# Performance work log

Hardware: AMD Instinct MI355X
Metric: run time of the kernel (lower is better)

## Reference

```python
import math
import jax, jax.numpy as jnp
import numpy as np

D_MODEL = 256
NUM_HEAD = 8
NUM_LEVEL = 1
KERNEL = 5
NUM_POINT = KERNEL * KERNEL
NUM_VAR = 5  # with_rotation=True
HEAD_DIM = D_MODEL // NUM_HEAD


def _kernel_indices(k=KERNEL):
    # odd kernel: linspace(-(k-1)/2, (k-1)/2, k); torch.meshgrid default 'ij'; stack([j,i])/k
    idx = jnp.linspace(-(k - 1) / 2.0, (k - 1) / 2.0, k)
    ii, jj = jnp.meshgrid(idx, idx, indexing='ij')
    return jnp.stack([jj, ii], axis=-1).reshape(-1, 2) / k  # (P, 2)


def setup_inputs() -> dict:
    key = jax.random.key(0)
    ks = jax.random.split(key, 8)
    B, LQ = 2, 4096
    Hf, Wf = 188, 188
    LV = Hf * Wf
    d = D_MODEL
    nb = NUM_LEVEL * NUM_HEAD * NUM_VAR
    na = NUM_HEAD * NUM_LEVEL * NUM_POINT
    return {
        'query': jax.random.normal(ks[0], (B, LQ, d), jnp.float32),
        'value': jax.random.normal(ks[1], (B, LV, d), jnp.float32),
        'ref_windows': jax.random.uniform(ks[2], (B, LQ, 7), jnp.float32),
        'W_box': jax.random.normal(ks[3], (nb, d), jnp.float32) * 0.02,
        'b_box': jax.random.uniform(ks[4], (nb,), jnp.float32),
        'W_attn': jax.random.normal(ks[5], (na, d), jnp.float32) * 0.02,
        'b_attn': jnp.zeros((na,), jnp.float32),
        'W_value': jax.random.normal(ks[6], (d, d), jnp.float32) * 0.02,
        'b_value': jnp.zeros((d,), jnp.float32),
        'W_out': jax.random.normal(ks[7], (d, d), jnp.float32) * 0.02,
        'b_out': jnp.zeros((d,), jnp.float32),
        'H_feat': Hf,
        'W_feat': Wf,
    }


def reference(query, value, ref_windows, W_box, b_box, W_attn, b_attn,
              W_value, b_value, W_out, b_out, H_feat, W_feat):
    B, LQ, d = query.shape
    LV = value.shape[1]
    Hh, Lv, P, Dh = NUM_HEAD, NUM_LEVEL, NUM_POINT, HEAD_DIM

    # value projection -> (B, LV, Hh, Dh)
    v = (value @ W_value.T + b_value).reshape(B, LV, Hh, Dh)

    # attention weights: softmax over (level*point) per head
    attn = jax.nn.softmax((query @ W_attn.T + b_attn).reshape(B, LQ, Hh, Lv * P), axis=-1)
    attn = attn.reshape(B, LQ, Hh, Lv, P)

    # --- _where_to_attend ---
    ob = (query @ W_box.T + b_box).reshape(B, LQ, Hh, Lv, NUM_VAR)
    rw = ref_windows[:, :, None, None, :]                    # (B,LQ,1,1,7)
    ref_boxes = rw[..., jnp.array([0, 1, 3, 4])]             # cx, cy, w, h
    ref_angles = rw[..., 6:7]
    off_boxes, off_angles = ob[..., :4], ob[..., 4:5]
    angles = (ref_angles + off_angles / 16.0) * (2.0 * math.pi)
    boxes = ref_boxes + off_boxes / 8.0 * ref_boxes[..., jnp.array([2, 3, 2, 3])]
    center = boxes[..., None, :2]                            # (B,LQ,Hh,Lv,1,2)
    size = boxes[..., None, 2:4]
    cos_a, sin_a = jnp.cos(angles), jnp.sin(angles)
    rot = jnp.stack([cos_a, -sin_a, sin_a, cos_a], axis=-1).reshape(B, LQ, Hh, Lv, 1, 2, 2)
    g = _kernel_indices() * jax.nn.relu(size)                # (B,LQ,Hh,Lv,P,2)
    grid = center + (g[..., None, :] * rot).sum(-1)          # (B,LQ,Hh,Lv,P,2), normalized [0,1]

    # --- single-level bilinear sampling (align_corners=False, zero padding) ---
    gl = grid[:, :, :, 0]                                    # (B,LQ,Hh,P,2)
    gx = gl[..., 0] * W_feat - 0.5
    gy = gl[..., 1] * H_feat - 0.5
    x0 = jnp.floor(gx)
    y0 = jnp.floor(gy)
    x0i = x0.astype(jnp.int32)
    y0i = y0.astype(jnp.int32)
    wx1 = gx - x0
    wy1 = gy - y0
    wx0 = 1.0 - wx1
    wy0 = 1.0 - wy1

    b_idx = jnp.arange(B)[:, None, None, None]
    h_idx = jnp.arange(Hh)[None, None, :, None]

    def gather(yi, xi):
        valid = (xi >= 0) & (xi < W_feat) & (yi >= 0) & (yi < H_feat)
        lin = jnp.clip(yi, 0, H_feat - 1) * W_feat + jnp.clip(xi, 0, W_feat - 1)
        return v[b_idx, lin, h_idx] * valid[..., None]       # (B,LQ,Hh,P,Dh)

    s = (gather(y0i, x0i) * (wy0 * wx0)[..., None]
         + gather(y0i, x0i + 1) * (wy0 * wx1)[..., None]
         + gather(y0i + 1, x0i) * (wy1 * wx0)[..., None]
         + gather(y0i + 1, x0i + 1) * (wy1 * wx1)[..., None])

    out_heads = (s * attn[:, :, :, 0, :, None]).sum(axis=3)  # (B,LQ,Hh,Dh)
    out = out_heads.reshape(B, LQ, Hh * Dh) @ W_out.T + b_out
    attn_w = attn.reshape(B, LQ, Hh, Lv, KERNEL, KERNEL)
    return out, attn_w
```

## Files before the change

### kernel.cpp

```cpp
#include <hip/hip_runtime.h>


typedef float floatx4 __attribute__((ext_vector_type(4)));
typedef short shortx8 __attribute__((ext_vector_type(8)));

static __device__ __forceinline__ unsigned short f2bf(float x) {
    unsigned int u = __float_as_uint(x);
    return (unsigned short)((u + 0x7fffu + ((u >> 16) & 1u)) >> 16);
}
static __device__ __forceinline__ unsigned int pack2(float a, float b) {
    return (unsigned int)f2bf(a) | ((unsigned int)f2bf(b) << 16);
}
static __device__ __forceinline__ void async16(const void* g, void* lds) {
    __builtin_amdgcn_global_load_lds(
        (const __attribute__((address_space(1))) unsigned int*)g,
        (__attribute__((address_space(3))) unsigned int*)lds, 16, 0, 0);
}

__global__ __launch_bounds__(256) void convert_kernel(
    const float* __restrict__ W_value, unsigned short* __restrict__ wvbf,
    const float* __restrict__ W_attn, const float* __restrict__ W_box,
    float* __restrict__ Wab,
    const float* __restrict__ W_out, unsigned short* __restrict__ wobf,
    const float* __restrict__ b_attn, const float* __restrict__ b_box,
    float* __restrict__ bab)
{
    const int blk = blockIdx.x, tid = threadIdx.x;
    if (blk < 16) {
        int base = blk * 1024 + tid;
#pragma unroll
        for (int k = 0; k < 4; ++k) {
            int j = base + k * 256;
            float4 f = ((const float4*)W_value)[j];
            ((uint2*)wvbf)[j] = make_uint2(pack2(f.x, f.y), pack2(f.z, f.w));
        }
    } else if (blk < 32) {
        int base = (blk - 16) * 1024 + tid;
#pragma unroll
        for (int k = 0; k < 4; ++k) {
            int j = base + k * 256;
            int row = j >> 6, col = (j & 63) * 4;
            float4 f;
            if (row < 200)      f = *(const float4*)(W_attn + (size_t)row * 256 + col);
            else if (row < 240) f = *(const float4*)(W_box + (size_t)(row - 200) * 256 + col);
            else                f = make_float4(0.f, 0.f, 0.f, 0.f);
            ((float4*)Wab)[j] = f;
        }
    } else if (blk < 48) {
        int base = (blk - 32) * 1024 + tid;
#pragma unroll
        for (int k = 0; k < 4; ++k) {
            int j = base + k * 256;
            float4 f = ((const float4*)W_out)[j];
            ((uint2*)wobf)[j] = make_uint2(pack2(f.x, f.y), pack2(f.z, f.w));
        }
    } else {
        bab[tid] = tid < 200 ? b_attn[tid] : (tid < 240 ? b_box[tid - 200] : 0.f);
    }
}

__global__ __launch_bounds__(512) void gemm_vproj(
    const float* __restrict__ A,
    const unsigned short* __restrict__ Bw,
    const float* __restrict__ bias,
    unsigned short* __restrict__ Vout, int M, int LV)
{
    __shared__ unsigned short Bs[256 * 264];
    const int tid = threadIdx.x;
    const int wv = tid >> 6, lane = tid & 63;
    const int lr = lane & 15, lq = lane >> 4;
    const int wn = wv & 3, wm = wv >> 2;

#pragma unroll
    for (int it = 0; it < 16; ++it) {
        int j = it * 512 + tid;
        int row = j >> 5, gc = j & 31;
        uint4 v = *(const uint4*)(Bw + (size_t)row * 256 + gc * 8);
        *(uint4*)((char*)Bs + row * 528 + gc * 16) = v;
    }
    __syncthreads();

    int bbase[4];
#pragma unroll
    for (int t = 0; t < 4; ++t) {
        int rb = wn * 64 + t * 16 + lr;
        bbase[t] = rb * 528 + lq * 16;
    }

    const int niter = (M + 63) / 64;
    for (int it = blockIdx.x; it < niter; it += gridDim.x) {
        const float* ap[2];
#pragma unroll
        for (int t = 0; t < 2; ++t) {
            int ra = it * 64 + wm * 32 + t * 16 + lr;
            ra = ra < M ? ra : M - 1;
            ap[t] = A + (size_t)ra * 256 + lq * 8;
        }
        floatx4 acc[2][4];
#pragma unroll
        for (int i = 0; i < 2; ++i)
#pragma unroll
            for (int j = 0; j < 4; ++j) acc[i][j] = (floatx4){0.f, 0.f, 0.f, 0.f};

#pragma unroll
        for (int ks = 0; ks < 8; ++ks) {
            shortx8 af[2], bf[4];
#pragma unroll
            for (int t = 0; t < 4; ++t)
                bf[t] = *(const shortx8*)((const char*)Bs + bbase[t] + ks * 64);
#pragma unroll
            for (int t = 0; t < 2; ++t) {
                float4 f0 = *(const float4*)(ap[t] + ks * 32);
                float4 f1 = *(const float4*)(ap[t] + ks * 32 + 4);
                union { uint4 u; shortx8 s; } cv;
                cv.u = make_uint4(pack2(f0.x, f0.y), pack2(f0.z, f0.w),
                                  pack2(f1.x, f1.y), pack2(f1.z, f1.w));
                af[t] = cv.s;
            }
#pragma unroll
            for (int ti = 0; ti < 2; ++ti)
#pragma unroll
                for (int tj = 0; tj < 4; ++tj)
                    acc[ti][tj] = __builtin_amdgcn_mfma_f32_16x16x32_bf16(bf[tj], af[ti], acc[ti][tj], 0, 0, 0);
        }
#pragma unroll
        for (int ti = 0; ti < 2; ++ti) {
            int m = it * 64 + wm * 32 + ti * 16 + lr;
            if (m >= M) continue;
            int b = m >= LV ? 1 : 0;
            int lv = m - (b ? LV : 0);
#pragma unroll
            for (int tj = 0; tj < 4; ++tj) {
                int nb = wn * 64 + tj * 16 + lq * 4;
                float4 bv = *(const float4*)(bias + nb);
                int h = nb >> 5, dh = nb & 31;
                unsigned short* dst = Vout + ((size_t)(b * 8 + h) * LV + lv) * 32 + dh;
                *(uint2*)dst = make_uint2(pack2(acc[ti][tj][0] + bv.x, acc[ti][tj][1] + bv.y),
                                          pack2(acc[ti][tj][2] + bv.z, acc[ti][tj][3] + bv.w));
            }
        }
    }
}

__global__ __launch_bounds__(256) void gemm_out(
    const unsigned short* __restrict__ Ab,
    const unsigned short* __restrict__ Bw,
    const float* __restrict__ bias,
    float* __restrict__ C, int M)
{
    constexpr int BM = 64;
    constexpr int NI = BM / 32, TI = BM / 32;
    __shared__ unsigned short As[2][BM * 64];
    __shared__ unsigned short Bs[2][128 * 64];
    const int tid = threadIdx.x;
    const int wv = tid >> 6, lane = tid & 63;
    const int lr = lane & 15, lq = lane >> 4;
    const int m0 = blockIdx.x * BM, n0 = blockIdx.y * 128;
    const int wm = wv & 1, wn = wv >> 1;
    const int srow = tid >> 3;
    const int colg = tid & 7;
    const int colgSw = colg ^ (srow & 7);

    floatx4 acc[TI][4];
#pragma unroll
    for (int i = 0; i < TI; ++i)
#pragma unroll
        for (int j = 0; j < 4; ++j) acc[i][j] = (floatx4){0.f, 0.f, 0.f, 0.f};

    auto compute = [&](const unsigned short* Acur, const unsigned short* Bcur) {
#pragma unroll
        for (int kb = 0; kb < 2; ++kb) {
            shortx8 af[TI], bfr[4];
#pragma unroll
            for (int t = 0; t < TI; ++t) {
                int arow = wm * (BM / 2) + t * 16 + lr;
                af[t] = *(const shortx8*)&Acur[arow * 64 + (((kb * 4 + lq) ^ (arow & 7)) * 8)];
            }
#pragma unroll
            for (int t = 0; t < 4; ++t) {
                int brow = wn * 64 + t * 16 + lr;
                bfr[t] = *(const shortx8*)&Bcur[brow * 64 + (((kb * 4 + lq) ^ (brow & 7)) * 8)];
            }
#pragma unroll
            for (int ti = 0; ti < TI; ++ti)
#pragma unroll
                for (int tj = 0; tj < 4; ++tj)
                    acc[ti][tj] = __builtin_amdgcn_mfma_f32_16x16x32_bf16(bfr[tj], af[ti], acc[ti][tj], 0, 0, 0);
        }
    };

#pragma unroll
    for (int i = 0; i < NI; ++i) {
        int ra = m0 + i * 32 + srow; ra = ra < M ? ra : M - 1;
        async16(Ab + (size_t)ra * 256 + colgSw * 8, (char*)As[0] + i * 4096 + wv * 1024);
    }
#pragma unroll
    for (int i = 0; i < 4; ++i) {
        int rb = n0 + i * 32 + srow;
        async16(Bw + (size_t)rb * 256 + colgSw * 8, (char*)Bs[0] + i * 4096 + wv * 1024);
    }
    __syncthreads();
    int cur = 0;
    for (int kc = 0; kc < 4; ++kc) {
        const int nk = (kc + 1) * 64;
        if (kc < 3) {
#pragma unroll
            for (int i = 0; i < NI; ++i) {
                int ra = m0 + i * 32 + srow; ra = ra < M ? ra : M - 1;
                async16(Ab + (size_t)ra * 256 + nk + colgSw * 8,
                        (char*)As[cur ^ 1] + i * 4096 + wv * 1024);
            }
#pragma unroll
            for (int i = 0; i < 4; ++i) {
                int rb = n0 + i * 32 + srow;
                async16(Bw + (size_t)rb * 256 + nk + colgSw * 8,
                        (char*)Bs[cur ^ 1] + i * 4096 + wv * 1024);
            }
        }
        compute(As[cur], Bs[cur]);
        __syncthreads();
        cur ^= 1;
    }
#pragma unroll
    for (int ti = 0; ti < TI; ++ti) {
        int m = m0 + wm * (BM / 2) + ti * 16 + lr;
        if (m >= M) continue;
        float* Crow = C + (size_t)m * 256;
#pragma unroll
        for (int tj = 0; tj < 4; ++tj) {
            int nb = n0 + wn * 64 + tj * 16 + lq * 4;
            float4 bv = *(const float4*)(bias + nb);
            float4 o = make_float4(acc[ti][tj][0] + bv.x, acc[ti][tj][1] + bv.y,
                                   acc[ti][tj][2] + bv.z, acc[ti][tj][3] + bv.w);
            *(float4*)(Crow + nb) = o;
        }
    }
}

__global__ __launch_bounds__(256) void gemm_nt_bias(
    const float* __restrict__ A, const float* __restrict__ W,
    const float* __restrict__ bias, float* __restrict__ C, int M)
{
    const int K = 256, N = 256;
    __shared__ float As[16][68];
    __shared__ float Bs[16][68];
    int tid = threadIdx.x;
    int tcol = tid & 15, trow = tid >> 4;
    int m0 = blockIdx.x * 64, n0 = blockIdx.y * 64;
    int lr = tid >> 2, lc = (tid & 3) << 2;
    float acc[4][4] = {};
    for (int k0 = 0; k0 < K; k0 += 16) {
        int arow = m0 + lr; if (arow > M - 1) arow = M - 1;
        float4 av = *(const float4*)(A + (size_t)arow * K + k0 + lc);
        float4 wv = *(const float4*)(W + (size_t)(n0 + lr) * K + k0 + lc);
        __syncthreads();
        As[lc + 0][lr] = av.x; As[lc + 1][lr] = av.y; As[lc + 2][lr] = av.z; As[lc + 3][lr] = av.w;
        Bs[lc + 0][lr] = wv.x; Bs[lc + 1][lr] = wv.y; Bs[lc + 2][lr] = wv.z; Bs[lc + 3][lr] = wv.w;
        __syncthreads();
#pragma unroll
        for (int k = 0; k < 16; ++k) {
            float4 a4 = *(const float4*)&As[k][trow << 2];
            float4 b4 = *(const float4*)&Bs[k][tcol << 2];
            float a[4] = {a4.x, a4.y, a4.z, a4.w};
            float bb[4] = {b4.x, b4.y, b4.z, b4.w};
#pragma unroll
            for (int i = 0; i < 4; i++)
#pragma unroll
                for (int j = 0; j < 4; j++) acc[i][j] += a[i] * bb[j];
        }
    }
#pragma unroll
    for (int i = 0; i < 4; i++) {
        int m = m0 + trow * 4 + i;
        if (m >= M) continue;
#pragma unroll
        for (int j = 0; j < 4; j++) {
            int n = n0 + tcol * 4 + j;
            C[(size_t)m * N + n] = acc[i][j] + bias[n];
        }
    }
}

__global__ __launch_bounds__(256) void decode_sample_kernel(
    const unsigned short* __restrict__ v,
    const float* __restrict__ logits,
    const float* __restrict__ ref_windows,
    float* __restrict__ attn_out,
    unsigned short* __restrict__ ohbf,
    const int* __restrict__ Hf_p, const int* __restrict__ Wf_p, int LV, int LQ)
{
    __shared__ float lg[8][32];
    __shared__ float rw[8][7];
    __shared__ float prm[8][6];
    __shared__ float mxinv[8][2];
    __shared__ uint4 pk[8][25][2];

    const int lin = blockIdx.y * 16 + blockIdx.x;
    const int nc = gridDim.y;
    const int seq = lin >> 3;
    const int c = seq % nc;
    const int s = (lin & 7) + ((seq / nc) << 3);
    const int b = s >> 3, h = s & 7;
    const int tid = threadIdx.x;
    const int Hf = *Hf_p, Wf = *Wf_p;
    const size_t mbase = (size_t)b * LQ + c * 8;

    if (tid < 240) {
        int qq = tid / 30, j = tid - qq * 30;
        int col = (j < 25) ? h * 25 + j : 200 + h * 5 + (j - 25);
        lg[qq][j] = logits[(mbase + qq) * 256 + col];
    }
    if (tid < 56) {
        int qq = tid / 7, k = tid - qq * 7;
        rw[qq][k] = ref_windows[(mbase + qq) * 7 + k];
    }
    __syncthreads();

    if (tid < 8) {
        int qq = tid;
        float mx = -1e30f;
#pragma unroll
        for (int p = 0; p < 25; p++) mx = fmaxf(mx, lg[qq][p]);
        float ssum = 0.f;
#pragma unroll
        for (int p = 0; p < 25; p++) ssum += expf(lg[qq][p] - mx);
        mxinv[qq][0] = mx; mxinv[qq][1] = 1.f / ssum;
        float cx = rw[qq][0] + lg[qq][25] * 0.125f * rw[qq][3];
        float cy = rw[qq][1] + lg[qq][26] * 0.125f * rw[qq][4];
        float bw = rw[qq][3] + lg[qq][27] * 0.125f * rw[qq][3];
        float bh = rw[qq][4] + lg[qq][28] * 0.125f * rw[qq][4];
        float ang = (rw[qq][6] + lg[qq][29] * 0.0625f) * 6.283185307179586f;
        prm[qq][0] = cx; prm[qq][1] = cy;
        prm[qq][2] = fmaxf(bw, 0.f); prm[qq][3] = fmaxf(bh, 0.f);
        prm[qq][4] = cosf(ang); prm[qq][5] = sinf(ang);
    }
    __syncthreads();

    if (tid < 200) {
        int qq = tid / 25, p = tid - qq * 25;
        float a = expf(lg[qq][p] - mxinv[qq][0]) * mxinv[qq][1];
        attn_out[(mbase + qq) * 200 + h * 25 + p] = a;
        int pi = p / 5, pj = p - pi * 5;
        float g0 = (float)(pj - 2) * 0.2f * prm[qq][2];
        float g1 = (float)(pi - 2) * 0.2f * prm[qq][3];
        float ca = prm[qq][4], sa = prm[qq][5];
        float gx = (prm[qq][0] + g0 * ca - g1 * sa) * (float)Wf - 0.5f;
        float gy = (prm[qq][1] + g0 * sa + g1 * ca) * (float)Hf - 0.5f;
        float x0f = floorf(gx), y0f = floorf(gy);
        int x0 = (int)x0f, y0 = (int)y0f;
        float wx1 = gx - x0f, wy1 = gy - y0f;
        float wx0 = 1.f - wx1, wy0 = 1.f - wy1;
        int y1 = y0 + 1;
        int bx; float wl, wr;
        if (x0 >= 0 && x0 <= Wf - 2)      { bx = x0;     wl = wx0; wr = wx1; }
        else if (x0 == -1)                { bx = 0;      wl = wx1; wr = 0.f; }
        else if (x0 == Wf - 1)            { bx = Wf - 2; wl = 0.f; wr = wx0; }
        else                              { bx = 0;      wl = 0.f; wr = 0.f; }
        float wy0v = (y0 >= 0 && y0 < Hf) ? wy0 : 0.f;
        float wy1v = (y1 >= 0 && y1 < Hf) ? wy1 : 0.f;
        int cy0 = min(max(y0, 0), Hf - 1), cy1 = min(max(y1, 0), Hf - 1);
        unsigned off0 = (unsigned)(cy0 * Wf + bx) * 16u;
        unsigned off1 = (unsigned)(cy1 * Wf + bx) * 16u;
        float aw0 = a * wy0v, aw1 = a * wy1v;
        pk[qq][p][0] = make_uint4(__float_as_uint(aw0 * wl), __float_as_uint(aw1 * wl), off0, off1);
        pk[qq][p][1] = make_uint4(__float_as_uint(aw0 * wr), __float_as_uint(aw1 * wr), off0, off1);
    }
    __syncthreads();

    const int qq = tid >> 5, l = tid & 31;
    const unsigned int* vw = (const unsigned int*)(v + (size_t)s * LV * 32);
    const uint4* pkp = &pk[qq][0][l >> 4];
    float e0 = 0.f, o0 = 0.f, e1 = 0.f, o1 = 0.f;
#pragma unroll
    for (int p = 0; p < 25; ++p) {
        uint4 t = pkp[2 * p];
        float w0 = __uint_as_float(t.x), w1 = __uint_as_float(t.y);
        unsigned u0 = vw[t.z + l];
        unsigned u1 = vw[t.w + l];
        e0 += w0 * __uint_as_float(u0 << 16);
        o0 += w0 * __uint_as_float(u0 & 0xffff0000u);
        e1 += w1 * __uint_as_float(u1 << 16);
        o1 += w1 * __uint_as_float(u1 & 0xffff0000u);
    }
    float a0 = e0 + e1, a1 = o0 + o1;
    a0 += __shfl_xor(a0, 16, 32);
    a1 += __shfl_xor(a1, 16, 32);
    if (l < 16)
        ((unsigned int*)ohbf)[(mbase + qq) * 128 + h * 16 + l] = pack2(a0, a1);
}

extern "C" void kernel_launch(void* const* d_in, const int* in_sizes, int n_in,
                              void* d_out, int out_size, void* d_ws, size_t ws_size,
                              hipStream_t stream) {
    const float* query       = (const float*)d_in[0];
    const float* value       = (const float*)d_in[1];
    const float* ref_windows = (const float*)d_in[2];
    const float* W_box       = (const float*)d_in[3];
    const float* b_box       = (const float*)d_in[4];
    const float* W_attn      = (const float*)d_in[5];
    const float* b_attn      = (const float*)d_in[6];
    const float* W_value     = (const float*)d_in[7];
    const float* b_value     = (const float*)d_in[8];
    const float* W_out       = (const float*)d_in[9];
    const float* b_out       = (const float*)d_in[10];
    const int*   Hf          = (const int*)d_in[11];
    const int*   Wf          = (const int*)d_in[12];

    const int M1 = in_sizes[1] / 256;
    const int MQ = in_sizes[0] / 256;
    const int LQ = MQ / 2;
    const int LV = M1 / 2;

    unsigned short* Vout = (unsigned short*)d_ws;
    unsigned short* ohbf = Vout + (size_t)M1 * 256;
    unsigned short* wvbf = ohbf + (size_t)MQ * 256;
    unsigned short* wobf = wvbf + 65536;
    float* Wab       = (float*)(wobf + 65536);
    float* bab       = Wab + 65536;
    float* logits    = bab + 256;

    float* out0     = (float*)d_out;
    float* attn_out = out0 + (size_t)MQ * 256;

    convert_kernel<<<49, 256, 0, stream>>>(W_value, wvbf, W_attn, W_box, Wab,
                                           W_out, wobf, b_attn, b_box, bab);
    gemm_vproj<<<256, 512, 0, stream>>>(value, wvbf, b_value, Vout, M1, LV);
    dim3 g2(MQ / 64, 4);
    gemm_nt_bias<<<g2, 256, 0, stream>>>(query, Wab, bab, logits, MQ);
    decode_sample_kernel<<<dim3(16, LQ / 8), 256, 0, stream>>>(
        Vout, logits, ref_windows, attn_out, ohbf, Hf, Wf, LV, LQ);
    dim3 g4(MQ / 64, 2);
    gemm_out<<<g4, 256, 0, stream>>>(ohbf, wobf, b_out, out0, MQ);
}
```

Baseline: 229.2 us.

## Stage value-projection A tiles in LDS with double-buffered register prefetch

The value-projection GEMM now converts each 64x64 fp32 A chunk to bf16 once per block and stages it in a swizzled, double-buffered LDS tile. The next chunk is prefetched into registers while MFMAs run on the current one. Before, each of the four N-waves loaded and converted its own A fragments straight from global memory. The resident W_value tile is now loaded with async global-to-LDS copies and an XOR swizzle instead of padded rows, and gemm_out is only moved within the file. The trade-off is an extra barrier per K chunk, more LDS use, and a reliance on the barrier waiting for the async B loads to finish.

```diff
diff --git a/kernel.cpp b/kernel.cpp
--- a/kernel.cpp
+++ b/kernel.cpp
@@ -65,37 +65,42 @@
     const float* __restrict__ bias,
     unsigned short* __restrict__ Vout, int M, int LV)
 {
-    __shared__ unsigned short Bs[256 * 264];
+    __shared__ unsigned short Bres[256 * 256];
+    __shared__ unsigned short As[2][64 * 64];
     const int tid = threadIdx.x;
     const int wv = tid >> 6, lane = tid & 63;
     const int lr = lane & 15, lq = lane >> 4;
-    const int wn = wv & 3, wm = wv >> 2;
-
-#pragma unroll
-    for (int it = 0; it < 16; ++it) {
-        int j = it * 512 + tid;
-        int row = j >> 5, gc = j & 31;
-        uint4 v = *(const uint4*)(Bw + (size_t)row * 256 + gc * 8);
-        *(uint4*)((char*)Bs + row * 528 + gc * 16) = v;
+    const int wm = wv & 1, wn = wv >> 1;
+    const int rowA = tid >> 3;
+    const int gA = tid & 7;
+    const int gAsw = gA ^ (rowA & 7);
+
+#pragma unroll
+    for (int j = 0; j < 16; ++j) {
+        int G = j * 512 + tid;
+        int row = G >> 5, g = G & 31;
+        async16(Bw + (size_t)row * 256 + (g ^ (row & 7)) * 8,
+                (char*)Bres + j * 8192 + wv * 1024);
+    }
+
+    const int niter = (M + 63) / 64;
+    const int stride = gridDim.x;
+
+    int it0 = blockIdx.x;
+    float4 pf0, pf1;
+    {
+        int ra = it0 * 64 + rowA; ra = ra < M ? ra : M - 1;
+        const float* ap = A + (size_t)ra * 256 + gA * 8;
+        pf0 = *(const float4*)ap; pf1 = *(const float4*)(ap + 4);
+        uint4 pv = make_uint4(pack2(pf0.x, pf0.y), pack2(pf0.z, pf0.w),
+                              pack2(pf1.x, pf1.y), pack2(pf1.z, pf1.w));
+        *(uint4*)((char*)As[0] + rowA * 128 + gAsw * 16) = pv;
     }
     __syncthreads();
 
-    int bbase[4];
-#pragma unroll
-    for (int t = 0; t < 4; ++t) {
-        int rb = wn * 64 + t * 16 + lr;
-        bbase[t] = rb * 528 + lq * 16;
-    }
-
-    const int niter = (M + 63) / 64;
-    for (int it = blockIdx.x; it < niter; it += gridDim.x) {
-        const float* ap[2];
-#pragma unroll
-        for (int t = 0; t < 2; ++t) {
-            int ra = it * 64 + wm * 32 + t * 16 + lr;
-            ra = ra < M ? ra : M - 1;
-            ap[t] = A + (size_t)ra * 256 + lq * 8;
-        }
+    int buf = 0;
+    for (int it = it0; it < niter; it += stride) {
+        const int m0 = it * 64;
         floatx4 acc[2][4];
 #pragma unroll
         for (int i = 0; i < 2; ++i)
@@ -103,29 +108,47 @@
             for (int j = 0; j < 4; ++j) acc[i][j] = (floatx4){0.f, 0.f, 0.f, 0.f};
 
 #pragma unroll
-        for (int ks = 0; ks < 8; ++ks) {
-            shortx8 af[2], bf[4];
-#pragma unroll
-            for (int t = 0; t < 4; ++t)
-                bf[t] = *(const shortx8*)((const char*)Bs + bbase[t] + ks * 64);
-#pragma unroll
-            for (int t = 0; t < 2; ++t) {
-                float4 f0 = *(const float4*)(ap[t] + ks * 32);
-                float4 f1 = *(const float4*)(ap[t] + ks * 32 + 4);
-                union { uint4 u; shortx8 s; } cv;
-                cv.u = make_uint4(pack2(f0.x, f0.y), pack2(f0.z, f0.w),
-                                  pack2(f1.x, f1.y), pack2(f1.z, f1.w));
-                af[t] = cv.s;
-            }
-#pragma unroll
-            for (int ti = 0; ti < 2; ++ti)
-#pragma unroll
-                for (int tj = 0; tj < 4; ++tj)
-                    acc[ti][tj] = __builtin_amdgcn_mfma_f32_16x16x32_bf16(bf[tj], af[ti], acc[ti][tj], 0, 0, 0);
+        for (int kc = 0; kc < 4; ++kc) {
+            int nit = it, nkc = kc + 1;
+            if (nkc == 4) { nkc = 0; nit = it + stride; if (nit >= niter) nit = it; }
+            {
+                int ra = nit * 64 + rowA; ra = ra < M ? ra : M - 1;
+                const float* ap = A + (size_t)ra * 256 + nkc * 64 + gA * 8;
+                pf0 = *(const float4*)ap; pf1 = *(const float4*)(ap + 4);
+            }
+#pragma unroll
+            for (int kb = 0; kb < 2; ++kb) {
+                shortx8 af[2], bfr[4];
+#pragma unroll
+                for (int t = 0; t < 2; ++t) {
+                    int arow = wm * 32 + t * 16 + lr;
+                    af[t] = *(const shortx8*)((const char*)As[buf] + arow * 128 +
+                                              (((kb * 4 + lq) ^ (arow & 7)) * 16));
+                }
+#pragma unroll
+                for (int t = 0; t < 4; ++t) {
+                    int brow = wn * 64 + t * 16 + lr;
+                    int gg = kc * 8 + kb * 4 + lq;
+                    bfr[t] = *(const shortx8*)((const char*)Bres + brow * 512 +
+                                               ((gg ^ (brow & 7)) * 16));
+                }
+#pragma unroll
+                for (int ti = 0; ti < 2; ++ti)
+#pragma unroll
+                    for (int tj = 0; tj < 4; ++tj)
+                        acc[ti][tj] = __builtin_amdgcn_mfma_f32_16x16x32_bf16(bfr[tj], af[ti], acc[ti][tj], 0, 0, 0);
+            }
+            {
+                uint4 pv = make_uint4(pack2(pf0.x, pf0.y), pack2(pf0.z, pf0.w),
+                                      pack2(pf1.x, pf1.y), pack2(pf1.z, pf1.w));
+                *(uint4*)((char*)As[buf ^ 1] + rowA * 128 + gAsw * 16) = pv;
+            }
+            __syncthreads();
+            buf ^= 1;
         }
 #pragma unroll
         for (int ti = 0; ti < 2; ++ti) {
-            int m = it * 64 + wm * 32 + ti * 16 + lr;
+            int m = m0 + wm * 32 + ti * 16 + lr;
             if (m >= M) continue;
             int b = m >= LV ? 1 : 0;
             int lv = m - (b ? LV : 0);
@@ -138,101 +161,6 @@
                 *(uint2*)dst = make_uint2(pack2(acc[ti][tj][0] + bv.x, acc[ti][tj][1] + bv.y),
                                           pack2(acc[ti][tj][2] + bv.z, acc[ti][tj][3] + bv.w));
             }
-        }
-    }
-}
-
-__global__ __launch_bounds__(256) void gemm_out(
-    const unsigned short* __restrict__ Ab,
-    const unsigned short* __restrict__ Bw,
-    const float* __restrict__ bias,
-    float* __restrict__ C, int M)
-{
-    constexpr int BM = 64;
-    constexpr int NI = BM / 32, TI = BM / 32;
-    __shared__ unsigned short As[2][BM * 64];
-    __shared__ unsigned short Bs[2][128 * 64];
-    const int tid = threadIdx.x;
-    const int wv = tid >> 6, lane = tid & 63;
-    const int lr = lane & 15, lq = lane >> 4;
-    const int m0 = blockIdx.x * BM, n0 = blockIdx.y * 128;
-    const int wm = wv & 1, wn = wv >> 1;
-    const int srow = tid >> 3;
-    const int colg = tid & 7;
-    const int colgSw = colg ^ (srow & 7);
-
-    floatx4 acc[TI][4];
-#pragma unroll
-    for (int i = 0; i < TI; ++i)
-#pragma unroll
-        for (int j = 0; j < 4; ++j) acc[i][j] = (floatx4){0.f, 0.f, 0.f, 0.f};
-
-    auto compute = [&](const unsigned short* Acur, const unsigned short* Bcur) {
-#pragma unroll
-        for (int kb = 0; kb < 2; ++kb) {
-            shortx8 af[TI], bfr[4];
-#pragma unroll
-            for (int t = 0; t < TI; ++t) {
-                int arow = wm * (BM / 2) + t * 16 + lr;
-                af[t] = *(const shortx8*)&Acur[arow * 64 + (((kb * 4 + lq) ^ (arow & 7)) * 8)];
-            }
-#pragma unroll
-            for (int t = 0; t < 4; ++t) {
-                int brow = wn * 64 + t * 16 + lr;
-                bfr[t] = *(const shortx8*)&Bcur[brow * 64 + (((kb * 4 + lq) ^ (brow & 7)) * 8)];
-            }
-#pragma unroll
-            for (int ti = 0; ti < TI; ++ti)
-#pragma unroll
-                for (int tj = 0; tj < 4; ++tj)
-                    acc[ti][tj] = __builtin_amdgcn_mfma_f32_16x16x32_bf16(bfr[tj], af[ti], acc[ti][tj], 0, 0, 0);
-        }
-    };
-
-#pragma unroll
-    for (int i = 0; i < NI; ++i) {
-        int ra = m0 + i * 32 + srow; ra = ra < M ? ra : M - 1;
-        async16(Ab + (size_t)ra * 256 + colgSw * 8, (char*)As[0] + i * 4096 + wv * 1024);
-    }
-#pragma unroll
-    for (int i = 0; i < 4; ++i) {
-        int rb = n0 + i * 32 + srow;
-        async16(Bw + (size_t)rb * 256 + colgSw * 8, (char*)Bs[0] + i * 4096 + wv * 1024);
-    }
-    __syncthreads();
-    int cur = 0;
-    for (int kc = 0; kc < 4; ++kc) {
-        const int nk = (kc + 1) * 64;
-        if (kc < 3) {
-#pragma unroll
-            for (int i = 0; i < NI; ++i) {
-                int ra = m0 + i * 32 + srow; ra = ra < M ? ra : M - 1;
-                async16(Ab + (size_t)ra * 256 + nk + colgSw * 8,
-                        (char*)As[cur ^ 1] + i * 4096 + wv * 1024);
-            }
-#pragma unroll
-            for (int i = 0; i < 4; ++i) {
-                int rb = n0 + i * 32 + srow;
-                async16(Bw + (size_t)rb * 256 + nk + colgSw * 8,
-                        (char*)Bs[cur ^ 1] + i * 4096 + wv * 1024);
-            }
-        }
-        compute(As[cur], Bs[cur]);
-        __syncthreads();
-        cur ^= 1;
-    }
-#pragma unroll
-    for (int ti = 0; ti < TI; ++ti) {
-        int m = m0 + wm * (BM / 2) + ti * 16 + lr;
-        if (m >= M) continue;
-        float* Crow = C + (size_t)m * 256;
-#pragma unroll
-        for (int tj = 0; tj < 4; ++tj) {
-            int nb = n0 + wn * 64 + tj * 16 + lq * 4;
-            float4 bv = *(const float4*)(bias + nb);
-            float4 o = make_float4(acc[ti][tj][0] + bv.x, acc[ti][tj][1] + bv.y,
-                                   acc[ti][tj][2] + bv.z, acc[ti][tj][3] + bv.w);
-            *(float4*)(Crow + nb) = o;
         }
     }
 }
@@ -389,6 +317,101 @@
         ((unsigned int*)ohbf)[(mbase + qq) * 128 + h * 16 + l] = pack2(a0, a1);
 }
 
+__global__ __launch_bounds__(256) void gemm_out(
+    const unsigned short* __restrict__ Ab,
+    const unsigned short* __restrict__ Bw,
+    const float* __restrict__ bias,
+    float* __restrict__ C, int M)
+{
+    constexpr int BM = 64;
+    constexpr int NI = BM / 32, TI = BM / 32;
+    __shared__ unsigned short As[2][BM * 64];
+    __shared__ unsigned short Bs[2][128 * 64];
+    const int tid = threadIdx.x;
+    const int wv = tid >> 6, lane = tid & 63;
+    const int lr = lane & 15, lq = lane >> 4;
+    const int m0 = blockIdx.x * BM, n0 = blockIdx.y * 128;
+    const int wm = wv & 1, wn = wv >> 1;
+    const int srow = tid >> 3;
+    const int colg = tid & 7;
+    const int colgSw = colg ^ (srow & 7);
+
+    floatx4 acc[TI][4];
+#pragma unroll
+    for (int i = 0; i < TI; ++i)
+#pragma unroll
+        for (int j = 0; j < 4; ++j) acc[i][j] = (floatx4){0.f, 0.f, 0.f, 0.f};
+
+    auto compute = [&](const unsigned short* Acur, const unsigned short* Bcur) {
+#pragma unroll
+        for (int kb = 0; kb < 2; ++kb) {
+            shortx8 af[TI], bfr[4];
+#pragma unroll
+            for (int t = 0; t < TI; ++t) {
+                int arow = wm * (BM / 2) + t * 16 + lr;
+                af[t] = *(const shortx8*)&Acur[arow * 64 + (((kb * 4 + lq) ^ (arow & 7)) * 8)];
+            }
+#pragma unroll
+            for (int t = 0; t < 4; ++t) {
+                int brow = wn * 64 + t * 16 + lr;
+                bfr[t] = *(const shortx8*)&Bcur[brow * 64 + (((kb * 4 + lq) ^ (brow & 7)) * 8)];
+            }
+#pragma unroll
+            for (int ti = 0; ti < TI; ++ti)
+#pragma unroll
+                for (int tj = 0; tj < 4; ++tj)
+                    acc[ti][tj] = __builtin_amdgcn_mfma_f32_16x16x32_bf16(bfr[tj], af[ti], acc[ti][tj], 0, 0, 0);
+        }
+    };
+
+#pragma unroll
+    for (int i = 0; i < NI; ++i) {
+        int ra = m0 + i * 32 + srow; ra = ra < M ? ra : M - 1;
+        async16(Ab + (size_t)ra * 256 + colgSw * 8, (char*)As[0] + i * 4096 + wv * 1024);
+    }
+#pragma unroll
+    for (int i = 0; i < 4; ++i) {
+        int rb = n0 + i * 32 + srow;
+        async16(Bw + (size_t)rb * 256 + colgSw * 8, (char*)Bs[0] + i * 4096 + wv * 1024);
+    }
+    __syncthreads();
+    int cur = 0;
+    for (int kc = 0; kc < 4; ++kc) {
+        const int nk = (kc + 1) * 64;
+        if (kc < 3) {
+#pragma unroll
+            for (int i = 0; i < NI; ++i) {
+                int ra = m0 + i * 32 + srow; ra = ra < M ? ra : M - 1;
+                async16(Ab + (size_t)ra * 256 + nk + colgSw * 8,
+                        (char*)As[cur ^ 1] + i * 4096 + wv * 1024);
+            }
+#pragma unroll
+            for (int i = 0; i < 4; ++i) {
+                int rb = n0 + i * 32 + srow;
+                async16(Bw + (size_t)rb * 256 + nk + colgSw * 8,
+                        (char*)Bs[cur ^ 1] + i * 4096 + wv * 1024);
+            }
+        }
+        compute(As[cur], Bs[cur]);
+        __syncthreads();
+        cur ^= 1;
+    }
+#pragma unroll
+    for (int ti = 0; ti < TI; ++ti) {
+        int m = m0 + wm * (BM / 2) + ti * 16 + lr;
+        if (m >= M) continue;
+        float* Crow = C + (size_t)m * 256;
+#pragma unroll
+        for (int tj = 0; tj < 4; ++tj) {
+            int nb = n0 + wn * 64 + tj * 16 + lq * 4;
+            float4 bv = *(const float4*)(bias + nb);
+            float4 o = make_float4(acc[ti][tj][0] + bv.x, acc[ti][tj][1] + bv.y,
+                                   acc[ti][tj][2] + bv.z, acc[ti][tj][3] + bv.w);
+            *(float4*)(Crow + nb) = o;
+        }
+    }
+}
+
 extern "C" void kernel_launch(void* const* d_in, const int* in_sizes, int n_in,
                               void* d_out, int out_size, void* d_ws, size_t ws_size,
                               hipStream_t stream) {
```

New measurement: 216.4 us. 5.6% less time.
